# Kernel optimization log

Hardware: AMD Instinct MI355X
Metric: run time of the kernel (lower is better)

The kernel has to match this reference:

```python
import jax, jax.numpy as jnp
import numpy as np

B, N, C = 2, 2048, 1536
H = 8
D = C // H  # 192, must match M's size


def setup_inputs() -> dict:
    key = jax.random.key(0)
    ks = jax.random.split(key, 5)
    x = jax.random.normal(ks[0], (B, N, C), dtype=jnp.float32)
    # nn.Linear(dim, 3*dim, bias=False): weight shape (3C, C)
    W_qkv = jax.random.normal(ks[1], (3 * C, C), dtype=jnp.float32) * (C ** -0.5)
    # nn.Linear(dim, dim) with bias
    W_proj = jax.random.normal(ks[2], (C, C), dtype=jnp.float32) * (C ** -0.5)
    b_proj = jnp.zeros((C,), dtype=jnp.float32)
    scale = jnp.asarray(D ** -0.5, dtype=jnp.float32)  # learned scalar, init head_dim**-0.5
    M = jnp.eye(D, dtype=jnp.float32)  # learned Mahalanobis metric, init identity
    return {"x": x, "W_qkv": W_qkv, "W_proj": W_proj, "b_proj": b_proj,
            "scale": scale, "M": M}


def reference(x, W_qkv, W_proj, b_proj, scale, M):
    Bv, Nv, Cv = x.shape
    qkv = x @ W_qkv.T                                  # [B,N,3C]
    qkv = qkv.reshape(Bv, Nv, 3, H, D).transpose(2, 0, 3, 1, 4)  # [3,B,H,N,D]
    q, k, v = qkv[0], qkv[1], qkv[2]
    q_M = q @ M                                        # [B,H,N,D]
    k_M = k @ M                                        # [B,H,N,D]
    qMq = jnp.sum(q * q_M, axis=-1, keepdims=True)     # [B,H,N,1]
    kMk = jnp.sum(k * k_M, axis=-1, keepdims=True)     # [B,H,N,1]
    kMk = jnp.swapaxes(kMk, -2, -1)                    # [B,H,1,N]
    qMk = jnp.einsum('bhnd,bhmd->bhnm', q_M, k)        # [B,H,N,N]
    dists = qMq + kMk - 2.0 * qMk                      # Mahalanobis quadratic form
    attn = jax.nn.softmax(-dists * scale, axis=-1)     # [B,H,N,N]
    out = jnp.einsum('bhnm,bhmd->bhnd', attn, v)       # [B,H,N,D]
    out = jnp.swapaxes(out, 1, 2).reshape(Bv, Nv, Cv)  # [B,N,C]
    out = out @ W_proj.T + b_proj
    return (out, attn, M)
```

## Files before the change

kernel.cpp:

```cpp
#include <hip/hip_runtime.h>

typedef _Float16 f16;
typedef __attribute__((ext_vector_type(8))) _Float16 f16x8;
typedef __attribute__((ext_vector_type(4))) float f32x4;

#define LOG2E 1.4426950408889634f
#define MFMA16(a, b, c) __builtin_amdgcn_mfma_f32_16x16x32_f16((a), (b), (c), 0, 0, 0)


__device__ __forceinline__ void gl16(const void* g, void* l) {
    __builtin_amdgcn_global_load_lds(
        (const __attribute__((address_space(1))) unsigned int*)g,
        (__attribute__((address_space(3))) unsigned int*)l, 16, 0, 0);
}

__global__ void k_cvt_all(const float* __restrict__ x, const float* __restrict__ wq,
                          const float* __restrict__ wp, f16* __restrict__ xh,
                          f16* __restrict__ wqh, f16* __restrict__ wph) {
    int i = blockIdx.x * 256 + threadIdx.x;
    const float4* s; short4* d; int off;
    if (i < 1572864) { s = (const float4*)x; d = (short4*)xh; off = i; }
    else if (i < 3342336) { s = (const float4*)wq; d = (short4*)wqh; off = i - 1572864; }
    else { s = (const float4*)wp; d = (short4*)wph; off = i - 3342336; }
    float4 v = s[off];
    union { f16 h[4]; short4 s4; } u;
    u.h[0] = (f16)v.x; u.h[1] = (f16)v.y; u.h[2] = (f16)v.z; u.h[3] = (f16)v.w;
    d[off] = u.s4;
}

__global__ void k_cvtM(const float* __restrict__ M, f16* __restrict__ Mt) {
    int i = blockIdx.x * 256 + threadIdx.x;
    if (i >= 192 * 192) return;
    int d = i / 192, e = i - (i / 192) * 192;
    Mt[d * 192 + e] = (f16)M[e * 192 + d];
}

__global__ __launch_bounds__(256) void k_gemm_qkv(
    const f16* __restrict__ A, const f16* __restrict__ Bw,
    f16* __restrict__ Qh, f16* __restrict__ Kh, f16* __restrict__ Vp)
{
    __shared__ __align__(16) char S[32768];
    const int tid = threadIdx.x, lane = tid & 63, w = tid >> 6;
    const int bid = blockIdx.x;
    const int xcd = bid & 7, cc = bid >> 3;
    const int mb = xcd * 4 + cc / 36, nb = cc - (cc / 36) * 36;
    const int m0 = mb * 128, n0 = nb * 128;
    const int sec = nb >= 24 ? 2 : (nb >= 12 ? 1 : 0);
    const int wm = (w & 1) * 64, wn = (w >> 1) * 64;
    const int L = lane & 15, g = lane >> 4;
    const char* Ab = (const char*)A;
    const char* Bb = (const char*)Bw;

    const char* gA[2]; const char* gB[2]; int ldso[2];
#pragma unroll
    for (int q = 0; q < 2; ++q) {
        int s = w * 128 + q * 64 + lane;
        int swz = ((s & 3) ^ ((s >> 2) & 3)) * 16;
        gA[q] = Ab + (size_t)(m0 + (s >> 2)) * 3072 + swz;
        gB[q] = Bb + (size_t)(n0 + (s >> 2)) * 3072 + swz;
        ldso[q] = w * 2048 + q * 1024;
    }
    const int gx = ((g ^ (L & 3)) << 4);

    f32x4 acc[4][4] = {};
#pragma unroll
    for (int q = 0; q < 2; ++q) {
        gl16(gA[q], S + ldso[q]);
        gl16(gB[q], S + 8192 + ldso[q]);
    }
    int buf = 0;
    for (int kk = 0; kk < 48; ++kk) {
        __syncthreads();
        if (kk < 47) {
            int nb_ = (buf ^ 1) * 16384;
#pragma unroll
            for (int q = 0; q < 2; ++q) {
                gl16(gA[q] + (kk + 1) * 64, S + nb_ + ldso[q]);
                gl16(gB[q] + (kk + 1) * 64, S + nb_ + 8192 + ldso[q]);
            }
        }
        const char* AsB = S + buf * 16384;
        const char* BsB = AsB + 8192;
        f16x8 af[4], bf[4];
#pragma unroll
        for (int i = 0; i < 4; ++i) {
            af[i] = *(const f16x8*)(AsB + (wm + i * 16 + L) * 64 + gx);
            bf[i] = *(const f16x8*)(BsB + (wn + i * 16 + L) * 64 + gx);
        }
        if (sec < 2) {
#pragma unroll
            for (int i = 0; i < 4; ++i)
#pragma unroll
                for (int j = 0; j < 4; ++j)
                    acc[i][j] = MFMA16(bf[j], af[i], acc[i][j]);
        } else {
#pragma unroll
            for (int i = 0; i < 4; ++i)
#pragma unroll
                for (int j = 0; j < 4; ++j)
                    acc[i][j] = MFMA16(af[i], bf[j], acc[i][j]);
        }
        buf ^= 1;
    }

    if (sec == 2) {
#pragma unroll
        for (int i = 0; i < 4; ++i)
#pragma unroll
            for (int j = 0; j < 4; ++j) {
                int rem = n0 + wn + j * 16 + L - 3072;
                int h = rem / 192, d = rem - h * 192;
                int gm = m0 + wm + i * 16 + g * 4;
                int gb = gm >> 11, nn = gm & 2047;
                union { f16 h4[4]; short4 s4; } u;
#pragma unroll
                for (int r = 0; r < 4; ++r) u.h4[r] = (f16)acc[i][j][r];
                int nnp = (nn & ~31) | (((nn >> 2) & 3) << 3) | (((nn >> 4) & 1) << 2) | (nn & 3);
                *(short4*)(Vp + (size_t)((gb * 8 + h) * 192 + d) * 2048 + nnp) = u.s4;
            }
    } else {
        f16* base = sec == 0 ? Qh : Kh;
#pragma unroll
        for (int i = 0; i < 4; ++i) {
            int gm = m0 + wm + i * 16 + L;
            int gb = gm >> 11, nn = gm & 2047;
#pragma unroll
            for (int j = 0; j < 4; ++j) {
                int rem = n0 + wn + j * 16 + g * 4 - sec * 1536;
                int h = rem / 192, d = rem - h * 192;
                union { f16 h4[4]; short4 s4; } u;
#pragma unroll
                for (int r = 0; r < 4; ++r) u.h4[r] = (f16)acc[i][j][r];
                *(short4*)(base + (size_t)((gb * 8 + h) * 2048 + nn) * 192 + d) = u.s4;
            }
        }
    }
}

__global__ __launch_bounds__(256) void k_mgemm(
    const f16* __restrict__ Qh, const f16* __restrict__ Kh,
    const f16* __restrict__ Mt, f16* __restrict__ QMh,
    const float* __restrict__ scale_p, float* __restrict__ qmq, float* __restrict__ kmk)
{
    const int tid = threadIdx.x, lane = tid & 63, w = tid >> 6;
    const int L = lane & 15, g = lane >> 4;
    const int isK = blockIdx.y;
    const f16* src = isK ? Kh : Qh;
    float* rowdot = isK ? kmk : qmq;
    const int row0 = blockIdx.x * 64 + w * 16;
    const int tokrow = row0 + L;
    f16x8 af[6];
#pragma unroll
    for (int ks = 0; ks < 6; ++ks)
        af[ks] = *(const f16x8*)((const char*)src + (size_t)tokrow * 384 + ks * 64 + g * 16);
    f32x4 acc[12] = {};
#pragma unroll
    for (int ct = 0; ct < 12; ++ct)
#pragma unroll
        for (int ks = 0; ks < 6; ++ks) {
            f16x8 bf = *(const f16x8*)((const char*)Mt + (ct * 16 + L) * 384 + ks * 64 + g * 16);
            acc[ct] = MFMA16(bf, af[ks], acc[ct]);
        }
    if (!isK) {
#pragma unroll
        for (int ct = 0; ct < 12; ++ct) {
            union { f16 h4[4]; short4 s4; } u;
#pragma unroll
            for (int r = 0; r < 4; ++r) u.h4[r] = (f16)acc[ct][r];
            *(short4*)(QMh + (size_t)tokrow * 192 + ct * 16 + g * 4) = u.s4;
        }
    }
    float s = 0.f;
#pragma unroll
    for (int ct = 0; ct < 12; ++ct) {
        union { short4 s4; f16 h[4]; } kv;
        kv.s4 = *(const short4*)(src + (size_t)tokrow * 192 + ct * 16 + g * 4);
#pragma unroll
        for (int r = 0; r < 4; ++r) s += acc[ct][r] * (float)kv.h[r];
    }
    s += __shfl_xor(s, 16); s += __shfl_xor(s, 32);
    if (lane < 16) rowdot[row0 + lane] = s * scale_p[0] * LOG2E;
}

__global__ __launch_bounds__(256) void k_attn(
    const f16* __restrict__ QMh, const f16* __restrict__ Kh,
    const f16* __restrict__ Vp, const float* __restrict__ kmk,
    const float* __restrict__ qmq, const float* __restrict__ scale_p,
    float* __restrict__ attn, f16* __restrict__ ctx, float* __restrict__ lrow)
{
    __shared__ __align__(16) char KsB[2][12288];
    __shared__ __align__(16) char VsB[2][15360];
    const int tid = threadIdx.x, lane = tid & 63, w = tid >> 6;
    const int L = lane & 15, g = lane >> 4;
    const int bx = blockIdx.x;
    const int bh = (bx & 7) * 2 + (bx >> 8);
    const int qb = (bx >> 3) & 31;
    const int row0 = qb * 64 + w * 16;
    const float a2 = 2.f * scale_p[0] * LOG2E;

    const char* qbase = (const char*)QMh + (size_t)(bh * 2048 + row0) * 384;
    f16x8 qf[6];
#pragma unroll
    for (int ks = 0; ks < 6; ++ks)
        qf[ks] = *(const f16x8*)(qbase + L * 384 + ks * 64 + g * 16);
    const char* Kb = (const char*)Kh + (size_t)bh * 2048 * 384;
    const char* Vb = (const char*)Vp + (size_t)bh * 192 * 4096;
    const float* kmkrow = kmk + bh * 2048;
    const float Crow = qmq[bh * 2048 + row0 + L];

    int ksrc[3], kdst[3], vsrc[3], vdst[3];
#pragma unroll
    for (int i = 0; i < 3; ++i) {
        int s = tid + 256 * i;
        int r = s / 24, c16 = s - r * 24;
        ksrc[i] = r * 384 + c16 * 16;
        kdst[i] = r * 384 + (((c16 & ~7) | ((c16 & 7) ^ (r & 7))) << 4);
        vsrc[i] = (s >> 2) * 4096 + (s & 3) * 16;
        vdst[i] = (s >> 2) * 80 + (s & 3) * 16;
    }
    int kslot[6];
#pragma unroll
    for (int ks = 0; ks < 6; ++ks) {
        int slot = ks * 4 + g;
        kslot[ks] = (((slot & ~7) | ((slot & 7) ^ (L & 7))) << 4);
    }

    int4 stk[3], stv[3];
#pragma unroll
    for (int i = 0; i < 3; ++i) {
        stk[i] = *(const int4*)(Kb + ksrc[i]);
        stv[i] = *(const int4*)(Vb + vsrc[i]);
    }
    f32x4 cacc[12] = {};
    float lacc = 0.f;
    float m_run = -3.0e38f, sc = 0.f;
    float* arow = attn + (size_t)(bh * 2048 + row0 + L) * 2048;

    for (int c = 0; c < 64; ++c) {
        char* Kl = KsB[c & 1];
        char* Vl = VsB[c & 1];
#pragma unroll
        for (int i = 0; i < 3; ++i) {
            *(int4*)(Kl + kdst[i]) = stk[i];
            *(int4*)(Vl + vdst[i]) = stv[i];
        }
        if (c < 63) {
#pragma unroll
            for (int i = 0; i < 3; ++i) {
                stk[i] = *(const int4*)(Kb + (size_t)(c + 1) * 12288 + ksrc[i]);
                stv[i] = *(const int4*)(Vb + (size_t)(c + 1) * 64 + vsrc[i]);
            }
        }
        __syncthreads();
        f32x4 a0 = {}, a1 = {};
#pragma unroll
        for (int ks = 0; ks < 6; ++ks) {
            f16x8 kf0 = *(const f16x8*)(Kl + L * 384 + kslot[ks]);
            f16x8 kf1 = *(const f16x8*)(Kl + (16 + L) * 384 + kslot[ks]);
            a0 = MFMA16(kf0, qf[ks], a0);
            a1 = MFMA16(kf1, qf[ks], a1);
        }
        float4 km0 = *(const float4*)(kmkrow + c * 32 + g * 4);
        float4 km1 = *(const float4*)(kmkrow + c * 32 + 16 + g * 4);
        float e8[8];
        e8[0] = a2 * a0[0] - km0.x - Crow;
        e8[1] = a2 * a0[1] - km0.y - Crow;
        e8[2] = a2 * a0[2] - km0.z - Crow;
        e8[3] = a2 * a0[3] - km0.w - Crow;
        e8[4] = a2 * a1[0] - km1.x - Crow;
        e8[5] = a2 * a1[1] - km1.y - Crow;
        e8[6] = a2 * a1[2] - km1.z - Crow;
        e8[7] = a2 * a1[3] - km1.w - Crow;
        float mx = fmaxf(fmaxf(fmaxf(e8[0], e8[1]), fmaxf(e8[2], e8[3])),
                         fmaxf(fmaxf(e8[4], e8[5]), fmaxf(e8[6], e8[7])));
        mx = fmaxf(mx, __shfl_xor(mx, 16));
        mx = fmaxf(mx, __shfl_xor(mx, 32));
        if (__any(mx > m_run + 4.f)) {
            float mnew = fmaxf(m_run, mx);
            float fr = __builtin_amdgcn_exp2f(m_run - mnew);
            lacc *= fr;
            float frc[4];
#pragma unroll
            for (int r = 0; r < 4; ++r) frc[r] = __shfl(fr, g * 4 + r);
#pragma unroll
            for (int dt = 0; dt < 12; ++dt)
#pragma unroll
                for (int r = 0; r < 4; ++r) cacc[dt][r] *= frc[r];
            m_run = mnew;
            sc = __builtin_amdgcn_exp2f(-m_run);
        }
        float p[8], ps[8];
#pragma unroll
        for (int j = 0; j < 8; ++j) {
            p[j] = __builtin_amdgcn_exp2f(e8[j]);
            ps[j] = p[j] * sc;
        }
        *(float4*)(arow + c * 32 + g * 4)      = make_float4(p[0], p[1], p[2], p[3]);
        *(float4*)(arow + c * 32 + 16 + g * 4) = make_float4(p[4], p[5], p[6], p[7]);
        lacc += ((ps[0] + ps[1]) + (ps[2] + ps[3])) + ((ps[4] + ps[5]) + (ps[6] + ps[7]));
        f16x8 pa;
        pa[0] = (f16)ps[0]; pa[1] = (f16)ps[1]; pa[2] = (f16)ps[2]; pa[3] = (f16)ps[3];
        pa[4] = (f16)ps[4]; pa[5] = (f16)ps[5]; pa[6] = (f16)ps[6]; pa[7] = (f16)ps[7];
#pragma unroll
        for (int dt = 0; dt < 12; ++dt) {
            f16x8 vf = *(const f16x8*)(Vl + (dt * 16 + L) * 80 + g * 16);
            cacc[dt] = MFMA16(pa, vf, cacc[dt]);
        }
    }
    lacc += __shfl_xor(lacc, 16);
    lacc += __shfl_xor(lacc, 32);
    if (g == 0) lrow[bh * 2048 + row0 + L] = __builtin_amdgcn_exp2f(-m_run) / lacc;
    float linv_r[4];
#pragma unroll
    for (int r = 0; r < 4; ++r) linv_r[r] = 1.f / __shfl(lacc, g * 4 + r);

    __syncthreads();
    char* scr = (char*)KsB + w * 6144;
#pragma unroll
    for (int dt = 0; dt < 12; ++dt)
#pragma unroll
        for (int r = 0; r < 4; ++r)
            *(f16*)(scr + (g * 4 + r) * 384 + (dt * 16 + L) * 2)
                = (f16)(cacc[dt][r] * linv_r[r]);
    const int b = bh >> 3, h = bh & 7;
#pragma unroll
    for (int t = 0; t < 6; ++t) {
        int chunk = t * 64 + lane;
        int tok = chunk / 24, c16 = chunk - tok * 24;
        int4 v = *(const int4*)(scr + tok * 384 + c16 * 16);
        *(int4*)((char*)ctx + ((size_t)(b * 2048 + row0 + tok) * 1536 + h * 192) * 2 + c16 * 16) = v;
    }
}

__global__ __launch_bounds__(256) void k_tail(
    const f16* __restrict__ A, const f16* __restrict__ Bw,
    const float* __restrict__ bias, float* __restrict__ out,
    float* __restrict__ attn, const float* __restrict__ lrow)
{
    const int tid = threadIdx.x;
    if (blockIdx.x >= 384) {
        const int row = (blockIdx.x - 384) * 8 + (tid >> 5);
        const int t = tid & 31;
        const float f = lrow[row];
        float* base = attn + (size_t)row * 2048;
#pragma unroll
        for (int i = 0; i < 16; ++i) {
            f32x4* p = (f32x4*)(base + i * 128) + t;
            f32x4 v = *p;
            v *= f;
            __builtin_nontemporal_store(v, p);
        }
        return;
    }
    __shared__ __align__(16) char S[32768];
    const int lane = tid & 63, w = tid >> 6;
    const int bid = blockIdx.x;
    const int xcd = bid & 7, cc = bid >> 3;
    const int mb = xcd * 4 + cc / 12, nbk = cc - (cc / 12) * 12;
    const int m0 = mb * 128, n0 = nbk * 128;
    const int wm = (w & 1) * 64, wn = (w >> 1) * 64;
    const int L = lane & 15, g = lane >> 4;
    const char* Ab = (const char*)A;
    const char* Bb = (const char*)Bw;

    const char* gA[2]; const char* gB[2]; int ldso[2];
#pragma unroll
    for (int q = 0; q < 2; ++q) {
        int s = w * 128 + q * 64 + lane;
        int swz = ((s & 3) ^ ((s >> 2) & 3)) * 16;
        gA[q] = Ab + (size_t)(m0 + (s >> 2)) * 3072 + swz;
        gB[q] = Bb + (size_t)(n0 + (s >> 2)) * 3072 + swz;
        ldso[q] = w * 2048 + q * 1024;
    }
    const int gx = ((g ^ (L & 3)) << 4);

    f32x4 acc[4][4] = {};
#pragma unroll
    for (int q = 0; q < 2; ++q) {
        gl16(gA[q], S + ldso[q]);
        gl16(gB[q], S + 8192 + ldso[q]);
    }
    int buf = 0;
    for (int kk = 0; kk < 48; ++kk) {
        __syncthreads();
        if (kk < 47) {
            int nb_ = (buf ^ 1) * 16384;
#pragma unroll
            for (int q = 0; q < 2; ++q) {
                gl16(gA[q] + (kk + 1) * 64, S + nb_ + ldso[q]);
                gl16(gB[q] + (kk + 1) * 64, S + nb_ + 8192 + ldso[q]);
            }
        }
        const char* AsB = S + buf * 16384;
        const char* BsB = AsB + 8192;
        f16x8 af[4], bf[4];
#pragma unroll
        for (int i = 0; i < 4; ++i) {
            af[i] = *(const f16x8*)(AsB + (wm + i * 16 + L) * 64 + gx);
            bf[i] = *(const f16x8*)(BsB + (wn + i * 16 + L) * 64 + gx);
        }
#pragma unroll
        for (int i = 0; i < 4; ++i)
#pragma unroll
            for (int j = 0; j < 4; ++j)
                acc[i][j] = MFMA16(bf[j], af[i], acc[i][j]);
        buf ^= 1;
    }
#pragma unroll
    for (int i = 0; i < 4; ++i) {
        int token = m0 + wm + i * 16 + L;
#pragma unroll
        for (int j = 0; j < 4; ++j) {
            int gnb = n0 + wn + j * 16 + g * 4;
            float4 bv = *(const float4*)(bias + gnb);
            float4 v = make_float4(acc[i][j][0] + bv.x, acc[i][j][1] + bv.y,
                                   acc[i][j][2] + bv.z, acc[i][j][3] + bv.w);
            *(float4*)(out + (size_t)token * 1536 + gnb) = v;
        }
    }
}

extern "C" void kernel_launch(void* const* d_in, const int* in_sizes, int n_in,
                              void* d_out, int out_size, void* d_ws, size_t ws_size,
                              hipStream_t stream)
{
    const float* x     = (const float*)d_in[0];
    const float* Wqkv  = (const float*)d_in[1];
    const float* Wproj = (const float*)d_in[2];
    const float* bproj = (const float*)d_in[3];
    const float* scale = (const float*)d_in[4];
    const float* M     = (const float*)d_in[5];
    float* out  = (float*)d_out;
    float* attn = out + 6291456;

    char* p = (char*)d_ws;
    f16* x_h     = (f16*)p;  p += 12582912;
    f16* Wqkv_h  = (f16*)p;  p += 14155776;
    f16* Wproj_h = (f16*)p;  p += 4718592;
    f16* Mt_h    = (f16*)p;  p += 73728;
    f16* Qh      = (f16*)p;  p += 12582912;
    f16* Kh      = (f16*)p;  p += 12582912;
    f16* Vp      = (f16*)p;  p += 12582912;
    f16* QMh     = (f16*)p;  p += 12582912;
    float* qmq   = (float*)p; p += 131072;
    float* kmk   = (float*)p; p += 131072;
    float* lrow  = (float*)p; p += 131072;
    f16* ctx     = (f16*)p;  p += 12582912;

    k_cvt_all<<<15360, 256, 0, stream>>>(x, Wqkv, Wproj, x_h, Wqkv_h, Wproj_h);
    k_cvtM<<<144, 256, 0, stream>>>(M, Mt_h);
    k_gemm_qkv<<<1152, 256, 0, stream>>>(x_h, Wqkv_h, Qh, Kh, Vp);
    k_mgemm<<<dim3(512, 2), 256, 0, stream>>>(Qh, Kh, Mt_h, QMh, scale, qmq, kmk);
    k_attn<<<512, 256, 0, stream>>>(QMh, Kh, Vp, kmk, qmq, scale, attn, ctx, lrow);
    k_tail<<<4480, 256, 0, stream>>>(ctx, Wproj_h, bproj, out, attn, lrow);
    hipMemcpyAsync(out + 73400320, M, 36864 * 4, hipMemcpyDeviceToDevice, stream);
}
```

Measured before the change: 415.6 us.

## Stage attention probabilities as fp16 with per-chunk scales, expand in tail

The attention kernel now writes unnormalized probabilities as fp16 into the first half of each output row, and records the running-max scale for each 32-column chunk in a new workspace buffer. The tail kernel then reads the fp16 values and the chunk scales, multiplies by the row normalizer, and expands in place to fp32 with nontemporal stores. This cuts the bytes written and re-read for the large attention matrix, in exchange for fp16 rounding of the probabilities and an extra scale buffer. It also raises wave priority around the MFMA loops with s_setprio.

```diff
diff --git a/kernel.cpp b/kernel.cpp
--- a/kernel.cpp
+++ b/kernel.cpp
@@ -186,7 +186,8 @@
     const f16* __restrict__ QMh, const f16* __restrict__ Kh,
     const f16* __restrict__ Vp, const float* __restrict__ kmk,
     const float* __restrict__ qmq, const float* __restrict__ scale_p,
-    float* __restrict__ attn, f16* __restrict__ ctx, float* __restrict__ lrow)
+    char* __restrict__ attnB, f16* __restrict__ ctx,
+    float* __restrict__ lrow, float* __restrict__ mcf)
 {
     __shared__ __align__(16) char KsB[2][12288];
     __shared__ __align__(16) char VsB[2][15360];
@@ -206,7 +207,8 @@
     const char* Kb = (const char*)Kh + (size_t)bh * 2048 * 384;
     const char* Vb = (const char*)Vp + (size_t)bh * 192 * 4096;
     const float* kmkrow = kmk + bh * 2048;
-    const float Crow = qmq[bh * 2048 + row0 + L];
+    const int rowi = bh * 2048 + row0 + L;
+    const float Crow = qmq[rowi];
 
     int ksrc[3], kdst[3], vsrc[3], vdst[3];
 #pragma unroll
@@ -233,8 +235,8 @@
     }
     f32x4 cacc[12] = {};
     float lacc = 0.f;
-    float m_run = -3.0e38f, sc = 0.f;
-    float* arow = attn + (size_t)(bh * 2048 + row0 + L) * 2048;
+    float m_run = -3.0e38f, scinv = 0.f;
+    char* arow16 = attnB + (size_t)rowi * 8192;
 
     for (int c = 0; c < 64; ++c) {
         char* Kl = KsB[c & 1];
@@ -253,6 +255,7 @@
         }
         __syncthreads();
         f32x4 a0 = {}, a1 = {};
+        __builtin_amdgcn_s_setprio(1);
 #pragma unroll
         for (int ks = 0; ks < 6; ++ks) {
             f16x8 kf0 = *(const f16x8*)(Kl + L * 384 + kslot[ks]);
@@ -260,6 +263,7 @@
             a0 = MFMA16(kf0, qf[ks], a0);
             a1 = MFMA16(kf1, qf[ks], a1);
         }
+        __builtin_amdgcn_s_setprio(0);
         float4 km0 = *(const float4*)(kmkrow + c * 32 + g * 4);
         float4 km1 = *(const float4*)(kmkrow + c * 32 + 16 + g * 4);
         float e8[8];
@@ -287,29 +291,30 @@
 #pragma unroll
                 for (int r = 0; r < 4; ++r) cacc[dt][r] *= frc[r];
             m_run = mnew;
-            sc = __builtin_amdgcn_exp2f(-m_run);
-        }
-        float p[8], ps[8];
-#pragma unroll
-        for (int j = 0; j < 8; ++j) {
-            p[j] = __builtin_amdgcn_exp2f(e8[j]);
-            ps[j] = p[j] * sc;
-        }
-        *(float4*)(arow + c * 32 + g * 4)      = make_float4(p[0], p[1], p[2], p[3]);
-        *(float4*)(arow + c * 32 + 16 + g * 4) = make_float4(p[4], p[5], p[6], p[7]);
+            scinv = __builtin_amdgcn_exp2f(m_run);
+        }
+        if (g == 0) mcf[(size_t)c * 32768 + rowi] = scinv;
+        float ps[8];
+#pragma unroll
+        for (int j = 0; j < 8; ++j)
+            ps[j] = __builtin_amdgcn_exp2f(e8[j] - m_run);
         lacc += ((ps[0] + ps[1]) + (ps[2] + ps[3])) + ((ps[4] + ps[5]) + (ps[6] + ps[7]));
-        f16x8 pa;
-        pa[0] = (f16)ps[0]; pa[1] = (f16)ps[1]; pa[2] = (f16)ps[2]; pa[3] = (f16)ps[3];
-        pa[4] = (f16)ps[4]; pa[5] = (f16)ps[5]; pa[6] = (f16)ps[6]; pa[7] = (f16)ps[7];
+        union { f16x8 v; short4 s4[2]; } pa;
+        pa.v[0] = (f16)ps[0]; pa.v[1] = (f16)ps[1]; pa.v[2] = (f16)ps[2]; pa.v[3] = (f16)ps[3];
+        pa.v[4] = (f16)ps[4]; pa.v[5] = (f16)ps[5]; pa.v[6] = (f16)ps[6]; pa.v[7] = (f16)ps[7];
+        *(short4*)(arow16 + c * 64 + g * 8)      = pa.s4[0];
+        *(short4*)(arow16 + c * 64 + 32 + g * 8) = pa.s4[1];
+        __builtin_amdgcn_s_setprio(1);
 #pragma unroll
         for (int dt = 0; dt < 12; ++dt) {
             f16x8 vf = *(const f16x8*)(Vl + (dt * 16 + L) * 80 + g * 16);
-            cacc[dt] = MFMA16(pa, vf, cacc[dt]);
-        }
+            cacc[dt] = MFMA16(pa.v, vf, cacc[dt]);
+        }
+        __builtin_amdgcn_s_setprio(0);
     }
     lacc += __shfl_xor(lacc, 16);
     lacc += __shfl_xor(lacc, 32);
-    if (g == 0) lrow[bh * 2048 + row0 + L] = __builtin_amdgcn_exp2f(-m_run) / lacc;
+    if (g == 0) lrow[rowi] = __builtin_amdgcn_exp2f(-m_run) / lacc;
     float linv_r[4];
 #pragma unroll
     for (int r = 0; r < 4; ++r) linv_r[r] = 1.f / __shfl(lacc, g * 4 + r);
@@ -335,20 +340,29 @@
 __global__ __launch_bounds__(256) void k_tail(
     const f16* __restrict__ A, const f16* __restrict__ Bw,
     const float* __restrict__ bias, float* __restrict__ out,
-    float* __restrict__ attn, const float* __restrict__ lrow)
+    char* __restrict__ attnB, const float* __restrict__ lrow,
+    const float* __restrict__ mcf)
 {
     const int tid = threadIdx.x;
     if (blockIdx.x >= 384) {
         const int row = (blockIdx.x - 384) * 8 + (tid >> 5);
         const int t = tid & 31;
-        const float f = lrow[row];
-        float* base = attn + (size_t)row * 2048;
+        const float lr = lrow[row];
+        char* slot = attnB + (size_t)row * 8192;
+        short4 s4[16];
+        float fc[16];
 #pragma unroll
         for (int i = 0; i < 16; ++i) {
-            f32x4* p = (f32x4*)(base + i * 128) + t;
-            f32x4 v = *p;
-            v *= f;
-            __builtin_nontemporal_store(v, p);
+            s4[i] = *(const short4*)(slot + t * 8 + i * 256);
+            fc[i] = mcf[(size_t)(i * 4 + (t >> 3)) * 32768 + row] * lr;
+        }
+        asm volatile("s_waitcnt vmcnt(0)" ::: "memory");
+#pragma unroll
+        for (int i = 0; i < 16; ++i) {
+            union { short4 v; f16 h[4]; } u; u.v = s4[i];
+            f32x4 o = { (float)u.h[0] * fc[i], (float)u.h[1] * fc[i],
+                        (float)u.h[2] * fc[i], (float)u.h[3] * fc[i] };
+            __builtin_nontemporal_store(o, (f32x4*)(slot + t * 16 + i * 512));
         }
         return;
     }
@@ -431,7 +445,7 @@
     const float* scale = (const float*)d_in[4];
     const float* M     = (const float*)d_in[5];
     float* out  = (float*)d_out;
-    float* attn = out + 6291456;
+    char* attnB = (char*)(out + 6291456);
 
     char* p = (char*)d_ws;
     f16* x_h     = (f16*)p;  p += 12582912;
@@ -445,13 +459,14 @@
     float* qmq   = (float*)p; p += 131072;
     float* kmk   = (float*)p; p += 131072;
     float* lrow  = (float*)p; p += 131072;
+    float* mcf   = (float*)p; p += 8388608;
     f16* ctx     = (f16*)p;  p += 12582912;
 
     k_cvt_all<<<15360, 256, 0, stream>>>(x, Wqkv, Wproj, x_h, Wqkv_h, Wproj_h);
     k_cvtM<<<144, 256, 0, stream>>>(M, Mt_h);
     k_gemm_qkv<<<1152, 256, 0, stream>>>(x_h, Wqkv_h, Qh, Kh, Vp);
     k_mgemm<<<dim3(512, 2), 256, 0, stream>>>(Qh, Kh, Mt_h, QMh, scale, qmq, kmk);
-    k_attn<<<512, 256, 0, stream>>>(QMh, Kh, Vp, kmk, qmq, scale, attn, ctx, lrow);
-    k_tail<<<4480, 256, 0, stream>>>(ctx, Wproj_h, bproj, out, attn, lrow);
+    k_attn<<<512, 256, 0, stream>>>(QMh, Kh, Vp, kmk, qmq, scale, attnB, ctx, lrow, mcf);
+    k_tail<<<4480, 256, 0, stream>>>(ctx, Wproj_h, bproj, out, attnB, lrow, mcf);
     hipMemcpyAsync(out + 73400320, M, 36864 * 4, hipMemcpyDeviceToDevice, stream);
 }
```

Result: faster. 388.8 us (-6.5%).
